# Performance work log

Hardware: AMD Instinct MI355X
Metric: run time of the kernel (lower is better)

The kernel has to match this reference:

```python
import jax, jax.numpy as jnp
import numpy as np

B, N, IN_DIM, OUT_DIM = 8, 2048, 256, 256
EDGE_P = 0.02   # adjacency density
MASK_P = 0.9    # fraction of valid nodes


def setup_inputs() -> dict:
    key = jax.random.key(0)
    ks = jax.random.split(key, 8)
    x = jax.random.normal(ks[0], (B, N, IN_DIM), dtype=jnp.float32)
    adj = (jax.random.uniform(ks[1], (B, N, N)) < EDGE_P).astype(jnp.float32)
    mask = (jax.random.uniform(ks[2], (B, N)) < MASK_P).astype(jnp.float32)
    # nn.Linear(in_dim, out_dim): W [out, in], b [out]
    lim1 = 1.0 / np.sqrt(IN_DIM)
    W = jax.random.uniform(ks[3], (OUT_DIM, IN_DIM), minval=-lim1, maxval=lim1, dtype=jnp.float32)
    b = jax.random.uniform(ks[4], (OUT_DIM,), minval=-lim1, maxval=lim1, dtype=jnp.float32)
    # nn.Linear(2*out_dim, 1): weight [1, 2D] split into a1 (acts on h_i), a2 (acts on h_j)
    lim2 = 1.0 / np.sqrt(2 * OUT_DIM)
    a1 = jax.random.uniform(ks[5], (OUT_DIM,), minval=-lim2, maxval=lim2, dtype=jnp.float32)
    a2 = jax.random.uniform(ks[6], (OUT_DIM,), minval=-lim2, maxval=lim2, dtype=jnp.float32)
    att_b = jax.random.uniform(ks[7], (), minval=-lim2, maxval=lim2, dtype=jnp.float32)
    return {"x": x, "adj": adj, "mask": mask, "W": W, "b": b, "a1": a1, "a2": a2, "att_b": att_b}


def reference(x, adj, mask, W, b, a1, a2, att_b):
    # h = Linear(x): [B, N, D]
    h = jnp.einsum('bni,di->bnd', x, W) + b
    # attention(cat([h_i, h_j])) == h_i @ a1 + h_j @ a2 + att_b (linear in each half)
    s1 = h @ a1  # [B, N] -> contributes along i
    s2 = h @ a2  # [B, N] -> contributes along j
    logits = s1[:, :, None] + s2[:, None, :] + att_b  # [B, N, N]
    att = jax.nn.sigmoid(logits) * adj
    att = att * mask[:, :, None] * mask[:, None, :]
    att = att / (jnp.sum(att, axis=-1, keepdims=True) + 1e-8)
    h_new = jnp.einsum('bij,bjd->bid', att, h)
    return h_new * mask[:, :, None]
```

## Files before the change

kernel.cpp:

```cpp
#include <hip/hip_runtime.h>
#include <hip/hip_bf16.h>

#define BB 8
#define NN 2048
#define DD 256
#define MM (BB * NN)

typedef __attribute__((ext_vector_type(8))) short bf16x8_t;
typedef __attribute__((ext_vector_type(4))) float f32x4_t;

__global__ __launch_bounds__(256) void gemm_h(
    const float* __restrict__ x,
    const float* __restrict__ Wt,
    const float* __restrict__ bias,
    __hip_bfloat16* __restrict__ h)
{
    __shared__ __hip_bfloat16 As[64][72];
    __shared__ __hip_bfloat16 Bs[64][72];

    const int tid  = threadIdx.x;
    const int r    = tid >> 2;
    const int cs   = (tid & 3) * 16;
    const int w    = tid >> 6;
    const int lane = tid & 63;
    const int m16  = lane & 15;
    const int quad = lane >> 4;
    const long rowBase = (long)blockIdx.x * 64;
    const int  colBase = blockIdx.y * 64;

    f32x4_t acc[4];
#pragma unroll
    for (int c = 0; c < 4; c++) acc[c] = (f32x4_t){0.f, 0.f, 0.f, 0.f};

    for (int k0 = 0; k0 < 256; k0 += 64) {
        const float4* ag = (const float4*)(x  + (rowBase + r) * 256 + k0 + cs);
        const float4* bg = (const float4*)(Wt + (long)(colBase + r) * 256 + k0 + cs);
        float4 av[4], bv[4];
#pragma unroll
        for (int q = 0; q < 4; q++) { av[q] = ag[q]; bv[q] = bg[q]; }

        __align__(16) __hip_bfloat16 ta[16], tb[16];
#pragma unroll
        for (int q = 0; q < 4; q++) {
            ta[q * 4 + 0] = __float2bfloat16(av[q].x);
            ta[q * 4 + 1] = __float2bfloat16(av[q].y);
            ta[q * 4 + 2] = __float2bfloat16(av[q].z);
            ta[q * 4 + 3] = __float2bfloat16(av[q].w);
            tb[q * 4 + 0] = __float2bfloat16(bv[q].x);
            tb[q * 4 + 1] = __float2bfloat16(bv[q].y);
            tb[q * 4 + 2] = __float2bfloat16(bv[q].z);
            tb[q * 4 + 3] = __float2bfloat16(bv[q].w);
        }

        __syncthreads();
        *(uint4*)&As[r][cs]     = *(uint4*)&ta[0];
        *(uint4*)&As[r][cs + 8] = *(uint4*)&ta[8];
        *(uint4*)&Bs[r][cs]     = *(uint4*)&tb[0];
        *(uint4*)&Bs[r][cs + 8] = *(uint4*)&tb[8];
        __syncthreads();

#pragma unroll
        for (int kk = 0; kk < 64; kk += 32) {
            bf16x8_t af = *(const bf16x8_t*)&As[w * 16 + m16][kk + quad * 8];
#pragma unroll
            for (int c = 0; c < 4; c++) {
                bf16x8_t bf = *(const bf16x8_t*)&Bs[c * 16 + m16][kk + quad * 8];
                acc[c] = __builtin_amdgcn_mfma_f32_16x16x32_bf16(af, bf, acc[c], 0, 0, 0);
            }
        }
    }

#pragma unroll
    for (int c = 0; c < 4; c++) {
        const int col = colBase + c * 16 + m16;
        const float bv = bias[col];
#pragma unroll
        for (int reg = 0; reg < 4; reg++) {
            const long row = rowBase + w * 16 + quad * 4 + reg;
            h[row * 256 + col] = __float2bfloat16(acc[c][reg] + bv);
        }
    }
}

struct __attribute__((aligned(8))) bf4 { __hip_bfloat16 v[4]; };

__global__ __launch_bounds__(256) void s_kernel(
    const __hip_bfloat16* __restrict__ h,
    const float* __restrict__ a1,
    const float* __restrict__ a2,
    const float* __restrict__ mask,
    const float* __restrict__ attb_p,
    float* __restrict__ s1b, float* __restrict__ t2)
{
    const int w = threadIdx.x >> 6;
    const int lane = threadIdx.x & 63;
    const long row = (long)blockIdx.x * 4 + w;

    bf4 hv = *(const bf4*)(h + row * 256 + lane * 4);
    float4 A1 = *(const float4*)(a1 + lane * 4);
    float4 A2 = *(const float4*)(a2 + lane * 4);
    const float h0 = __bfloat162float(hv.v[0]), h1 = __bfloat162float(hv.v[1]);
    const float h2 = __bfloat162float(hv.v[2]), h3 = __bfloat162float(hv.v[3]);
    float p1 = h0 * A1.x + h1 * A1.y + h2 * A1.z + h3 * A1.w;
    float p2 = h0 * A2.x + h1 * A2.y + h2 * A2.z + h3 * A2.w;
#pragma unroll
    for (int off = 32; off; off >>= 1) {
        p1 += __shfl_down(p1, off);
        p2 += __shfl_down(p2, off);
    }
    if (lane == 0) {
        s1b[row] = p1 + attb_p[0];
        t2[row]  = (mask[row] != 0.f) ? p2 : -1e30f;
    }
}

__global__ __launch_bounds__(256, 8) void attn_agg(
    const float* __restrict__ adj,
    const float* __restrict__ mask,
    const __hip_bfloat16* __restrict__ h,
    const float* __restrict__ s1b,
    const float* __restrict__ t2,
    float* __restrict__ out)
{
    __shared__ unsigned short s_j[2048];
    __shared__ float          s_w[2048];
    __shared__ float          s_part[4][DD];
    __shared__ int            s_cnt;
    __shared__ float          s_sum[4];

    const int tid  = threadIdx.x;
    const int wv   = tid >> 6;
    const int lane = tid & 63;
    const int b    = blockIdx.x & 7;
    const int i    = blockIdx.x >> 3;
    const long row   = (long)b * NN + i;
    const long mbase = (long)b * NN;

    const float mask_i = mask[row];
    if (mask_i == 0.f) {
        out[row * 256 + tid] = 0.f;
        return;
    }
    if (tid == 0) s_cnt = 0;
    __syncthreads();

    const float si = s1b[row];
    const float4* arow = (const float4*)(adj + row * NN);
    const float4* trow = (const float4*)(t2 + mbase);

    float4 A0 = arow[tid], A1 = arow[256 + tid];
    float4 T0 = trow[tid], T1 = trow[256 + tid];

    float lsum = 0.f;
#pragma unroll
    for (int g = 0; g < 2; g++) {
        const int jb = g * 1024 + tid * 4;
        const float av[4] = {g ? A1.x : A0.x, g ? A1.y : A0.y, g ? A1.z : A0.z, g ? A1.w : A0.w};
        const float tv[4] = {g ? T1.x : T0.x, g ? T1.y : T0.y, g ? T1.z : T0.z, g ? T1.w : T0.w};
#pragma unroll
        for (int e = 0; e < 4; e++) {
            const float z   = si + tv[e];
            const float sig = __builtin_amdgcn_rcpf(1.f + __expf(-z));
            const float wgt = av[e] * sig;
            lsum += wgt;
            if (wgt != 0.f) {
                const int pos = atomicAdd(&s_cnt, 1);
                s_j[pos] = (unsigned short)(jb + e);
                s_w[pos] = wgt;
            }
        }
    }

#pragma unroll
    for (int off = 32; off; off >>= 1) lsum += __shfl_down(lsum, off);
    if (lane == 0) s_sum[wv] = lsum;
    __syncthreads();

    const float inv = 1.f / (s_sum[0] + s_sum[1] + s_sum[2] + s_sum[3] + 1e-8f);
    const int   cnt = s_cnt;

    const int qs = ((cnt + 15) >> 4) << 2;
    const int ks = min(wv * qs, cnt);
    const int ke = min(ks + qs, cnt);
    const char* hb   = (const char*)(h + mbase * 256);
    const int   loff = lane * 8;

    float c0 = 0.f, c1 = 0.f, c2 = 0.f, c3 = 0.f;
    int k = ks;
    for (; k + 8 <= ke; k += 8) {
        ushort4 ja = *(const ushort4*)&s_j[k];
        ushort4 jb2 = *(const ushort4*)&s_j[k + 4];
        float4  wa = *(const float4*)&s_w[k];
        float4  wb = *(const float4*)&s_w[k + 4];
        uint2 u[8];
        u[0] = *(const uint2*)(hb + ((int)ja.x  << 9) + loff);
        u[1] = *(const uint2*)(hb + ((int)ja.y  << 9) + loff);
        u[2] = *(const uint2*)(hb + ((int)ja.z  << 9) + loff);
        u[3] = *(const uint2*)(hb + ((int)ja.w  << 9) + loff);
        u[4] = *(const uint2*)(hb + ((int)jb2.x << 9) + loff);
        u[5] = *(const uint2*)(hb + ((int)jb2.y << 9) + loff);
        u[6] = *(const uint2*)(hb + ((int)jb2.z << 9) + loff);
        u[7] = *(const uint2*)(hb + ((int)jb2.w << 9) + loff);
        const float ww[8] = {wa.x, wa.y, wa.z, wa.w, wb.x, wb.y, wb.z, wb.w};
#pragma unroll
        for (int q = 0; q < 8; q++) {
            c0 += ww[q] * __uint_as_float(u[q].x << 16);
            c1 += ww[q] * __uint_as_float(u[q].x & 0xffff0000u);
            c2 += ww[q] * __uint_as_float(u[q].y << 16);
            c3 += ww[q] * __uint_as_float(u[q].y & 0xffff0000u);
        }
    }
    for (; k + 4 <= ke; k += 4) {
        ushort4 ja = *(const ushort4*)&s_j[k];
        float4  wa = *(const float4*)&s_w[k];
        uint2 u[4];
        u[0] = *(const uint2*)(hb + ((int)ja.x << 9) + loff);
        u[1] = *(const uint2*)(hb + ((int)ja.y << 9) + loff);
        u[2] = *(const uint2*)(hb + ((int)ja.z << 9) + loff);
        u[3] = *(const uint2*)(hb + ((int)ja.w << 9) + loff);
        const float ww[4] = {wa.x, wa.y, wa.z, wa.w};
#pragma unroll
        for (int q = 0; q < 4; q++) {
            c0 += ww[q] * __uint_as_float(u[q].x << 16);
            c1 += ww[q] * __uint_as_float(u[q].x & 0xffff0000u);
            c2 += ww[q] * __uint_as_float(u[q].y << 16);
            c3 += ww[q] * __uint_as_float(u[q].y & 0xffff0000u);
        }
    }
    for (; k < ke; k++) {
        const int jj = s_j[k];
        const float wk = s_w[k];
        uint2 u = *(const uint2*)(hb + (jj << 9) + loff);
        c0 += wk * __uint_as_float(u.x << 16);
        c1 += wk * __uint_as_float(u.x & 0xffff0000u);
        c2 += wk * __uint_as_float(u.y << 16);
        c3 += wk * __uint_as_float(u.y & 0xffff0000u);
    }

    *(float4*)&s_part[wv][lane * 4] = make_float4(c0, c1, c2, c3);
    __syncthreads();

    const float total = s_part[0][tid] + s_part[1][tid] + s_part[2][tid] + s_part[3][tid];
    out[row * 256 + tid] = total * inv;
}

extern "C" void kernel_launch(void* const* d_in, const int* in_sizes, int n_in,
                              void* d_out, int out_size, void* d_ws, size_t ws_size,
                              hipStream_t stream) {
    const float* x    = (const float*)d_in[0];
    const float* adj  = (const float*)d_in[1];
    const float* mask = (const float*)d_in[2];
    const float* W    = (const float*)d_in[3];
    const float* bias = (const float*)d_in[4];
    const float* a1   = (const float*)d_in[5];
    const float* a2   = (const float*)d_in[6];
    const float* attb = (const float*)d_in[7];
    float* out = (float*)d_out;

    __hip_bfloat16* h = (__hip_bfloat16*)d_ws;
    float* s1b = (float*)((char*)d_ws + (size_t)MM * DD * 2);
    float* t2  = s1b + MM;

    gemm_h<<<dim3(MM / 64, DD / 64), 256, 0, stream>>>(x, W, bias, h);
    s_kernel<<<MM / 4, 256, 0, stream>>>(h, a1, a2, mask, attb, s1b, t2);
    attn_agg<<<MM, 256, 0, stream>>>(adj, mask, h, s1b, t2, out);
}
```

Before: 239.8 us.

## Process several rows per attention block and prefetch the next adjacency row

The aggregation kernel now handles 8 consecutive rows per block instead of one. The t2 row is loaded once and reused for all 8 rows. While the current row is being processed, the next row's adjacency values and mask are loaded into registers, so the global-memory latency of the adjacency stream overlaps with sigmoid, compaction and gather work. In exchange the grid is 8x smaller and each block's rows run one after another, which reduces parallelism across blocks and raises register pressure.

New measurement: 253.1 us. 1.06x slower.

```diff
diff --git a/kernel.cpp b/kernel.cpp
--- a/kernel.cpp
+++ b/kernel.cpp
@@ -5,6 +5,7 @@
 #define NN 2048
 #define DD 256
 #define MM (BB * NN)
+#define RPB 8
 
 typedef __attribute__((ext_vector_type(8))) short bf16x8_t;
 typedef __attribute__((ext_vector_type(4))) float f32x4_t;
@@ -125,123 +126,142 @@
     __shared__ unsigned short s_j[2048];
     __shared__ float          s_w[2048];
     __shared__ float          s_part[4][DD];
-    __shared__ int            s_cnt;
+    __shared__ int            s_cnt[RPB];
     __shared__ float          s_sum[4];
 
     const int tid  = threadIdx.x;
     const int wv   = tid >> 6;
     const int lane = tid & 63;
     const int b    = blockIdx.x & 7;
-    const int i    = blockIdx.x >> 3;
-    const long row   = (long)b * NN + i;
+    const int ibase = (blockIdx.x >> 3) * RPB;
     const long mbase = (long)b * NN;
-
-    const float mask_i = mask[row];
-    if (mask_i == 0.f) {
-        out[row * 256 + tid] = 0.f;
-        return;
-    }
-    if (tid == 0) s_cnt = 0;
+    const char* hb = (const char*)(h + mbase * 256);
+
+    if (tid < RPB) s_cnt[tid] = 0;
+
+    const float4* trow = (const float4*)(t2 + mbase);
+    const float4 T0 = trow[tid], T1 = trow[256 + tid];
+
+    const float4* arow = (const float4*)(adj + (mbase + ibase) * NN);
+
+    float  cmask = mask[mbase + ibase];
+    float4 cA0, cA1;
+    if (cmask != 0.f) { cA0 = arow[tid]; cA1 = arow[256 + tid]; }
     __syncthreads();
 
-    const float si = s1b[row];
-    const float4* arow = (const float4*)(adj + row * NN);
-    const float4* trow = (const float4*)(t2 + mbase);
-
-    float4 A0 = arow[tid], A1 = arow[256 + tid];
-    float4 T0 = trow[tid], T1 = trow[256 + tid];
-
-    float lsum = 0.f;
-#pragma unroll
-    for (int g = 0; g < 2; g++) {
-        const int jb = g * 1024 + tid * 4;
-        const float av[4] = {g ? A1.x : A0.x, g ? A1.y : A0.y, g ? A1.z : A0.z, g ? A1.w : A0.w};
-        const float tv[4] = {g ? T1.x : T0.x, g ? T1.y : T0.y, g ? T1.z : T0.z, g ? T1.w : T0.w};
-#pragma unroll
-        for (int e = 0; e < 4; e++) {
-            const float z   = si + tv[e];
-            const float sig = __builtin_amdgcn_rcpf(1.f + __expf(-z));
-            const float wgt = av[e] * sig;
-            lsum += wgt;
-            if (wgt != 0.f) {
-                const int pos = atomicAdd(&s_cnt, 1);
-                s_j[pos] = (unsigned short)(jb + e);
-                s_w[pos] = wgt;
-            }
-        }
-    }
-
-#pragma unroll
-    for (int off = 32; off; off >>= 1) lsum += __shfl_down(lsum, off);
-    if (lane == 0) s_sum[wv] = lsum;
-    __syncthreads();
-
-    const float inv = 1.f / (s_sum[0] + s_sum[1] + s_sum[2] + s_sum[3] + 1e-8f);
-    const int   cnt = s_cnt;
-
-    const int qs = ((cnt + 15) >> 4) << 2;
-    const int ks = min(wv * qs, cnt);
-    const int ke = min(ks + qs, cnt);
-    const char* hb   = (const char*)(h + mbase * 256);
-    const int   loff = lane * 8;
-
-    float c0 = 0.f, c1 = 0.f, c2 = 0.f, c3 = 0.f;
-    int k = ks;
-    for (; k + 8 <= ke; k += 8) {
-        ushort4 ja = *(const ushort4*)&s_j[k];
-        ushort4 jb2 = *(const ushort4*)&s_j[k + 4];
-        float4  wa = *(const float4*)&s_w[k];
-        float4  wb = *(const float4*)&s_w[k + 4];
-        uint2 u[8];
-        u[0] = *(const uint2*)(hb + ((int)ja.x  << 9) + loff);
-        u[1] = *(const uint2*)(hb + ((int)ja.y  << 9) + loff);
-        u[2] = *(const uint2*)(hb + ((int)ja.z  << 9) + loff);
-        u[3] = *(const uint2*)(hb + ((int)ja.w  << 9) + loff);
-        u[4] = *(const uint2*)(hb + ((int)jb2.x << 9) + loff);
-        u[5] = *(const uint2*)(hb + ((int)jb2.y << 9) + loff);
-        u[6] = *(const uint2*)(hb + ((int)jb2.z << 9) + loff);
-        u[7] = *(const uint2*)(hb + ((int)jb2.w << 9) + loff);
-        const float ww[8] = {wa.x, wa.y, wa.z, wa.w, wb.x, wb.y, wb.z, wb.w};
-#pragma unroll
-        for (int q = 0; q < 8; q++) {
-            c0 += ww[q] * __uint_as_float(u[q].x << 16);
-            c1 += ww[q] * __uint_as_float(u[q].x & 0xffff0000u);
-            c2 += ww[q] * __uint_as_float(u[q].y << 16);
-            c3 += ww[q] * __uint_as_float(u[q].y & 0xffff0000u);
-        }
-    }
-    for (; k + 4 <= ke; k += 4) {
-        ushort4 ja = *(const ushort4*)&s_j[k];
-        float4  wa = *(const float4*)&s_w[k];
-        uint2 u[4];
-        u[0] = *(const uint2*)(hb + ((int)ja.x << 9) + loff);
-        u[1] = *(const uint2*)(hb + ((int)ja.y << 9) + loff);
-        u[2] = *(const uint2*)(hb + ((int)ja.z << 9) + loff);
-        u[3] = *(const uint2*)(hb + ((int)ja.w << 9) + loff);
-        const float ww[4] = {wa.x, wa.y, wa.z, wa.w};
-#pragma unroll
-        for (int q = 0; q < 4; q++) {
-            c0 += ww[q] * __uint_as_float(u[q].x << 16);
-            c1 += ww[q] * __uint_as_float(u[q].x & 0xffff0000u);
-            c2 += ww[q] * __uint_as_float(u[q].y << 16);
-            c3 += ww[q] * __uint_as_float(u[q].y & 0xffff0000u);
-        }
-    }
-    for (; k < ke; k++) {
-        const int jj = s_j[k];
-        const float wk = s_w[k];
-        uint2 u = *(const uint2*)(hb + (jj << 9) + loff);
-        c0 += wk * __uint_as_float(u.x << 16);
-        c1 += wk * __uint_as_float(u.x & 0xffff0000u);
-        c2 += wk * __uint_as_float(u.y << 16);
-        c3 += wk * __uint_as_float(u.y & 0xffff0000u);
-    }
-
-    *(float4*)&s_part[wv][lane * 4] = make_float4(c0, c1, c2, c3);
-    __syncthreads();
-
-    const float total = s_part[0][tid] + s_part[1][tid] + s_part[2][tid] + s_part[3][tid];
-    out[row * 256 + tid] = total * inv;
+    for (int r = 0; r < RPB; r++) {
+        float  nmask = 0.f;
+        float4 nA0, nA1;
+        if (r + 1 < RPB) {
+            nmask = mask[mbase + ibase + r + 1];
+            if (nmask != 0.f) {
+                nA0 = arow[(r + 1) * 512 + tid];
+                nA1 = arow[(r + 1) * 512 + 256 + tid];
+            }
+        }
+
+        const long row = mbase + ibase + r;
+        if (cmask != 0.f) {
+            const float si = s1b[row];
+            float lsum = 0.f;
+#pragma unroll
+            for (int g = 0; g < 2; g++) {
+                const int jb = g * 1024 + tid * 4;
+                const float av[4] = {g ? cA1.x : cA0.x, g ? cA1.y : cA0.y,
+                                     g ? cA1.z : cA0.z, g ? cA1.w : cA0.w};
+                const float tv[4] = {g ? T1.x : T0.x, g ? T1.y : T0.y,
+                                     g ? T1.z : T0.z, g ? T1.w : T0.w};
+#pragma unroll
+                for (int e = 0; e < 4; e++) {
+                    const float z   = si + tv[e];
+                    const float sig = __builtin_amdgcn_rcpf(1.f + __expf(-z));
+                    const float wgt = av[e] * sig;
+                    lsum += wgt;
+                    if (wgt != 0.f) {
+                        const int pos = atomicAdd(&s_cnt[r], 1);
+                        s_j[pos] = (unsigned short)(jb + e);
+                        s_w[pos] = wgt;
+                    }
+                }
+            }
+
+#pragma unroll
+            for (int off = 32; off; off >>= 1) lsum += __shfl_down(lsum, off);
+            if (lane == 0) s_sum[wv] = lsum;
+            __syncthreads();
+
+            const float inv = 1.f / (s_sum[0] + s_sum[1] + s_sum[2] + s_sum[3] + 1e-8f);
+            const int   cnt = s_cnt[r];
+
+            const int qs = ((cnt + 15) >> 4) << 2;
+            const int ks = min(wv * qs, cnt);
+            const int ke = min(ks + qs, cnt);
+            const int loff = lane * 8;
+
+            float c0 = 0.f, c1 = 0.f, c2 = 0.f, c3 = 0.f;
+            int k = ks;
+            for (; k + 8 <= ke; k += 8) {
+                ushort4 ja  = *(const ushort4*)&s_j[k];
+                ushort4 jb2 = *(const ushort4*)&s_j[k + 4];
+                float4  wa  = *(const float4*)&s_w[k];
+                float4  wb  = *(const float4*)&s_w[k + 4];
+                uint2 u[8];
+                u[0] = *(const uint2*)(hb + ((int)ja.x  << 9) + loff);
+                u[1] = *(const uint2*)(hb + ((int)ja.y  << 9) + loff);
+                u[2] = *(const uint2*)(hb + ((int)ja.z  << 9) + loff);
+                u[3] = *(const uint2*)(hb + ((int)ja.w  << 9) + loff);
+                u[4] = *(const uint2*)(hb + ((int)jb2.x << 9) + loff);
+                u[5] = *(const uint2*)(hb + ((int)jb2.y << 9) + loff);
+                u[6] = *(const uint2*)(hb + ((int)jb2.z << 9) + loff);
+                u[7] = *(const uint2*)(hb + ((int)jb2.w << 9) + loff);
+                const float ww[8] = {wa.x, wa.y, wa.z, wa.w, wb.x, wb.y, wb.z, wb.w};
+#pragma unroll
+                for (int q = 0; q < 8; q++) {
+                    c0 += ww[q] * __uint_as_float(u[q].x << 16);
+                    c1 += ww[q] * __uint_as_float(u[q].x & 0xffff0000u);
+                    c2 += ww[q] * __uint_as_float(u[q].y << 16);
+                    c3 += ww[q] * __uint_as_float(u[q].y & 0xffff0000u);
+                }
+            }
+            for (; k + 4 <= ke; k += 4) {
+                ushort4 ja = *(const ushort4*)&s_j[k];
+                float4  wa = *(const float4*)&s_w[k];
+                uint2 u[4];
+                u[0] = *(const uint2*)(hb + ((int)ja.x << 9) + loff);
+                u[1] = *(const uint2*)(hb + ((int)ja.y << 9) + loff);
+                u[2] = *(const uint2*)(hb + ((int)ja.z << 9) + loff);
+                u[3] = *(const uint2*)(hb + ((int)ja.w << 9) + loff);
+                const float ww[4] = {wa.x, wa.y, wa.z, wa.w};
+#pragma unroll
+                for (int q = 0; q < 4; q++) {
+                    c0 += ww[q] * __uint_as_float(u[q].x << 16);
+                    c1 += ww[q] * __uint_as_float(u[q].x & 0xffff0000u);
+                    c2 += ww[q] * __uint_as_float(u[q].y << 16);
+                    c3 += ww[q] * __uint_as_float(u[q].y & 0xffff0000u);
+                }
+            }
+            for (; k < ke; k++) {
+                const int jj = s_j[k];
+                const float wk = s_w[k];
+                uint2 u = *(const uint2*)(hb + (jj << 9) + loff);
+                c0 += wk * __uint_as_float(u.x << 16);
+                c1 += wk * __uint_as_float(u.x & 0xffff0000u);
+                c2 += wk * __uint_as_float(u.y << 16);
+                c3 += wk * __uint_as_float(u.y & 0xffff0000u);
+            }
+
+            *(float4*)&s_part[wv][lane * 4] = make_float4(c0, c1, c2, c3);
+            __syncthreads();
+
+            const float total = s_part[0][tid] + s_part[1][tid]
+                              + s_part[2][tid] + s_part[3][tid];
+            out[row * 256 + tid] = total * inv;
+        } else {
+            out[row * 256 + tid] = 0.f;
+        }
+
+        cmask = nmask; cA0 = nA0; cA1 = nA1;
+    }
 }
 
 extern "C" void kernel_launch(void* const* d_in, const int* in_sizes, int n_in,
@@ -263,5 +283,5 @@
 
     gemm_h<<<dim3(MM / 64, DD / 64), 256, 0, stream>>>(x, W, bias, h);
     s_kernel<<<MM / 4, 256, 0, stream>>>(h, a1, a2, mask, attb, s1b, t2);
-    attn_agg<<<MM, 256, 0, stream>>>(adj, mask, h, s1b, t2, out);
-}
+    attn_agg<<<MM / RPB, 256, 0, stream>>>(adj, mask, h, s1b, t2, out);
+}
```
